# Optimization experiments

Hardware: AMD Instinct MI355X
Metric: run time of the kernel (lower is better)

Reference implementation:

```python
import jax, jax.numpy as jnp
import numpy as np

B, T, D_MODEL = 2, 1024, 1024
HEAD_DIM = 128
NUM_HEADS = D_MODEL // HEAD_DIM          # 8
EXPAND_V = 1
HEAD_V = HEAD_DIM * EXPAND_V             # 128
KEY_DIM = NUM_HEADS * HEAD_DIM           # 1024
VALUE_DIM = NUM_HEADS * HEAD_V           # 1024
CONV_SIZE = 4
NUM_LEVELS = int(np.log2(T)) + 1         # 11 Fenwick levels
EPS = 1e-5
SCALE = HEAD_DIM ** -0.5


def setup_inputs() -> dict:
    ks = jax.random.split(jax.random.key(0), 20)
    w = lambda i, shp: 0.02 * jax.random.normal(ks[i], shp, jnp.float32)
    return {
        'x': jax.random.normal(ks[0], (B, T, D_MODEL), jnp.float32),
        'cos': jax.random.normal(ks[1], (T, HEAD_DIM), jnp.float32),
        'sin': jax.random.normal(ks[2], (T, HEAD_DIM), jnp.float32),
        'Wq': w(3, (D_MODEL, KEY_DIM)),
        'Wk': w(4, (D_MODEL, KEY_DIM)),
        'Wv': w(5, (D_MODEL, VALUE_DIM)),
        'Wb': w(6, (D_MODEL, NUM_HEADS)),
        'Wa': w(7, (D_MODEL, NUM_HEADS)),
        'Wl': w(8, (D_MODEL, NUM_HEADS * NUM_LEVELS)),
        'Wg': w(9, (D_MODEL, VALUE_DIM)),
        'Wo': w(10, (VALUE_DIM, D_MODEL)),
        'conv_q': 0.2 * jax.random.normal(ks[11], (KEY_DIM, CONV_SIZE), jnp.float32),
        'conv_k': 0.2 * jax.random.normal(ks[12], (KEY_DIM, CONV_SIZE), jnp.float32),
        'conv_v': 0.2 * jax.random.normal(ks[13], (VALUE_DIM, CONV_SIZE), jnp.float32),
        'A_log': jnp.log(jax.random.uniform(ks[14], (NUM_HEADS,), jnp.float32, 1.0, 16.0)),
        'dt_bias': jnp.log(jnp.expm1(jax.random.uniform(ks[15], (NUM_HEADS,), jnp.float32, 0.001, 0.1))),
        'norm_w': jnp.ones((HEAD_V,), jnp.float32),
    }


def _dwconv_silu(x, w):
    # causal depthwise conv1d (ShortConvolution, activation=silu). x:[B,T,C], w:[C,K]
    xp = jnp.pad(x, ((0, 0), (CONV_SIZE - 1, 0), (0, 0)))
    y = jax.lax.conv_general_dilated(xp, w.T[:, None, :], (1,), 'VALID',
                                     dimension_numbers=('NHC', 'HIO', 'NHC'),
                                     feature_group_count=w.shape[0])
    return jax.nn.silu(y)


def _l2norm(x):
    return x * jax.lax.rsqrt(jnp.sum(x * x, -1, keepdims=True) + 1e-6)


def _levels():
    # Fenwick-tree level of token s (0-indexed) in the prefix decomposition at time t:
    # level(t,s) = floor(log2((t+1) XOR s)) for s <= t.
    n = jnp.arange(1, T + 1, dtype=jnp.int32)[:, None]
    s = jnp.arange(T, dtype=jnp.int32)[None, :]
    xval = jnp.maximum(jnp.bitwise_xor(n, s), 1)
    lev = jnp.floor(jnp.log2(xval.astype(jnp.float32))).astype(jnp.int32)
    return jnp.clip(lev, 0, NUM_LEVELS - 1)  # [T,T]


def _forward(x, Wq, Wk, Wv, Wb, Wa, Wl, Wg, Wo, conv_q, conv_k, conv_v, A_log, dt_bias, norm_w):
    # projections + short conv + silu, split heads -> [B,H,T,d]
    q = _dwconv_silu(x @ Wq, conv_q).reshape(B, T, NUM_HEADS, HEAD_DIM).transpose(0, 2, 1, 3)
    k = _dwconv_silu(x @ Wk, conv_k).reshape(B, T, NUM_HEADS, HEAD_DIM).transpose(0, 2, 1, 3)
    v = _dwconv_silu(x @ Wv, conv_v).reshape(B, T, NUM_HEADS, HEAD_V).transpose(0, 2, 1, 3)
    q = _l2norm(q) * SCALE
    k = _l2norm(k)
    beta = jax.nn.sigmoid(x @ Wb).transpose(0, 2, 1)                      # [B,H,T]
    g = -jnp.exp(A_log) * jax.nn.softplus(x @ Wa + dt_bias)              # [B,T,H] log-decay per step
    gc = jnp.cumsum(g.transpose(0, 2, 1), axis=-1)                        # [B,H,T]
    lam = jax.nn.sigmoid(x @ Wl).reshape(B, T, NUM_HEADS, NUM_LEVELS).transpose(0, 2, 1, 3)  # [B,H,T,L]

    idx = jnp.arange(T)
    causal = idx[:, None] >= idx[None, :]
    strict = idx[:, None] > idx[None, :]
    # stable decay matrix D[t,s] = exp(gc_t - gc_s) <= 1 for s <= t
    logD = gc[..., :, None] - gc[..., None, :]
    Dm = jnp.exp(jnp.where(causal, logD, -jnp.inf))                       # [B,H,T,T]

    # WY / UT transform of the gated delta rule:
    #   u_t = beta_t * v_t - beta_t * sum_{s<t} (k_t . k_s) exp(gc_t-gc_s) u_s
    Akk = jnp.einsum('bhtd,bhsd->bhts', k, k) * Dm * strict
    u = jax.scipy.linalg.solve_triangular(beta[..., None] * Akk,
                                          beta[..., None] * v,
                                          lower=True, unit_diagonal=True)  # [B,H,T,dv]

    # log-linear (hierarchical) readout: o_t = sum_s lam_t[level(t,s)] * (q_t.k_s) D[t,s] * u_s
    P = jnp.einsum('bhtd,bhsd->bhts', q, k) * Dm
    M = jnp.take_along_axis(lam, _levels()[None, None], axis=3)           # [B,H,T,T]
    o = jnp.einsum('bhts,bhsd->bhtd', P * M, u).transpose(0, 2, 1, 3)      # [B,T,H,dv]

    # gated RMSNorm output gate, then output projection
    gate = (x @ Wg).reshape(B, T, NUM_HEADS, HEAD_V)
    o = o * jax.lax.rsqrt(jnp.mean(o * o, -1, keepdims=True) + EPS) * norm_w * jax.nn.silu(gate)
    return o.reshape(B, T, VALUE_DIM) @ Wo


def reference(x, cos, sin, Wq, Wk, Wv, Wb, Wa, Wl, Wg, Wo, conv_q, conv_k, conv_v, A_log, dt_bias, norm_w):
    # cos/sin are accepted (block signature) but unused, matching the source module.
    return _forward(x, Wq, Wk, Wv, Wb, Wa, Wl, Wg, Wo, conv_q, conv_k, conv_v, A_log, dt_bias, norm_w)
```

## Files before the change

### kernel.cpp

```cpp
#include <hip/hip_runtime.h>
#include <hip/hip_bf16.h>
#include <math.h>

#define SCALE_Q 0.08838834764831845f

typedef __bf16 bf16x8 __attribute__((ext_vector_type(8)));
typedef float f32x4 __attribute__((ext_vector_type(4)));

static __device__ __forceinline__ float sigm(float x){ return 1.f/(1.f+__expf(-x)); }
static __device__ __forceinline__ ushort f2b(float v){
  __hip_bfloat16 t = __float2bfloat16(v);
  return __builtin_bit_cast(ushort, t);
}
static __device__ __forceinline__ float b2f(ushort u){
  unsigned v = (unsigned)u << 16; return __builtin_bit_cast(float, v);
}

__global__ __launch_bounds__(256) void prep_all(const float* __restrict__ Wq,
    const float* __restrict__ Wk, const float* __restrict__ Wv,
    const float* __restrict__ Wg, const float* __restrict__ Wo,
    const float* __restrict__ X, const float* __restrict__ Wb,
    const float* __restrict__ Wa, const float* __restrict__ Wl,
    ushort* __restrict__ Wt4, ushort* __restrict__ Wot,
    ushort* __restrict__ x16, float* __restrict__ Wsm)
{
  int z = blockIdx.z;
  int tid = threadIdx.x;
  int flat = blockIdx.y * 32 + blockIdx.x;
  if (z < 5) {
    __shared__ float tile[32][36];
    const float* W = (z==0)?Wq:(z==1)?Wk:(z==2)?Wv:(z==3)?Wg:Wo;
    ushort* Wt = (z<4)? (Wt4 + (size_t)z*1048576) : Wot;
    int n0 = blockIdx.x*32, k0 = blockIdx.y*32;
    int r = tid >> 3, c4 = (tid & 7) << 2;
    *(float4*)&tile[r][c4] = *(const float4*)&W[(size_t)(k0 + r)*1024 + n0 + c4];
    __syncthreads();
    ushort4 o;
    o.x = f2b(tile[c4+0][r]); o.y = f2b(tile[c4+1][r]);
    o.z = f2b(tile[c4+2][r]); o.w = f2b(tile[c4+3][r]);
    *(ushort4*)&Wt[(size_t)(n0 + r)*1024 + k0 + c4] = o;
  } else if (z < 7) {
    int idx = (z-5)*262144 + flat*256 + tid;
    float4 v = *(const float4*)&X[(size_t)idx*4];
    ushort4 o; o.x=f2b(v.x); o.y=f2b(v.y); o.z=f2b(v.z); o.w=f2b(v.w);
    *(ushort4*)&x16[(size_t)idx*4] = o;
  } else {
    int idx = flat*256 + tid;
    if (idx < 1024*104) {
      int k = idx / 104, c = idx % 104;
      float v = (c < 8) ? Wb[k*8+c] : (c < 16) ? Wa[k*8+(c-8)] : Wl[k*88+(c-16)];
      Wsm[idx] = v;
    }
  }
}

__global__ __launch_bounds__(256) void gemm_bf16(const ushort* __restrict__ A,
    const ushort* __restrict__ Bt, void* __restrict__ C0, float* __restrict__ C1,
    int M, int N, int K, int nsplit, int ld0, int ld1, int c0bf16)
{
  __shared__ ushort As[3][128*32];
  __shared__ ushort Bs[3][128*32];
  int tid = threadIdx.x;
  int gx = gridDim.x;
  int nwg = gx * gridDim.y;
  int id = blockIdx.y * gx + blockIdx.x;
  int id2 = (id & 7) * (nwg >> 3) + (id >> 3);
  int bm = (id2 / gx) * 128, bn = (id2 % gx) * 128;
  int wave = tid >> 6, lane = tid & 63;
  int wm = (wave >> 1) * 64, wn = (wave & 1) * 64;
  int l16 = lane & 15, kh = lane >> 4;
  f32x4 acc[4][4] = {};
  int rowA0 = tid >> 2, boA = (tid & 3) * 16;
  int niter = K >> 5;

  #pragma unroll
  for (int s = 0; s < 2; ++s) {
    int k0 = s << 5;
    #pragma unroll
    for (int j = 0; j < 2; ++j) {
      int row = rowA0 + j*64;
      const char* gA = (const char*)A + (((size_t)(bm+row)*K + k0)*2 + boA);
      const char* gB = (const char*)Bt + (((size_t)(bn+row)*K + k0)*2 + boA);
      __builtin_amdgcn_global_load_lds((const __attribute__((address_space(1))) unsigned*)gA,
        (__attribute__((address_space(3))) unsigned*)((char*)&As[s][0] + row*64 + boA), 16, 0, 0);
      __builtin_amdgcn_global_load_lds((const __attribute__((address_space(1))) unsigned*)gB,
        (__attribute__((address_space(3))) unsigned*)((char*)&Bs[s][0] + row*64 + boA), 16, 0, 0);
    }
  }
  asm volatile("s_waitcnt vmcnt(4)" ::: "memory");
  __builtin_amdgcn_s_barrier();
  __builtin_amdgcn_sched_barrier(0);
  for (int i = 0; i < niter; ++i) {
    int cur = i % 3;
    if (i + 2 < niter) {
      int k0 = (i+2) << 5;
      int nb = (i+2) % 3;
      char* al = (char*)&As[nb][0];
      char* bl = (char*)&Bs[nb][0];
      #pragma unroll
      for (int j = 0; j < 2; ++j) {
        int row = rowA0 + j*64;
        const char* gA = (const char*)A + (((size_t)(bm+row)*K + k0)*2 + boA);
        const char* gB = (const char*)Bt + (((size_t)(bn+row)*K + k0)*2 + boA);
        __builtin_amdgcn_global_load_lds((const __attribute__((address_space(1))) unsigned*)gA,
          (__attribute__((address_space(3))) unsigned*)(al + row*64 + boA), 16, 0, 0);
        __builtin_amdgcn_global_load_lds((const __attribute__((address_space(1))) unsigned*)gB,
          (__attribute__((address_space(3))) unsigned*)(bl + row*64 + boA), 16, 0, 0);
      }
    }
    bf16x8 af[4], bfr[4];
    #pragma unroll
    for (int ii = 0; ii < 4; ++ii)
      af[ii] = *(bf16x8*)((char*)&As[cur][0] + (wm + ii*16 + l16)*64 + kh*16);
    #pragma unroll
    for (int j = 0; j < 4; ++j)
      bfr[j] = *(bf16x8*)((char*)&Bs[cur][0] + (wn + j*16 + l16)*64 + kh*16);
    #pragma unroll
    for (int ii = 0; ii < 4; ++ii)
      #pragma unroll
      for (int j = 0; j < 4; ++j)
        acc[ii][j] = __builtin_amdgcn_mfma_f32_16x16x32_bf16(af[ii], bfr[j], acc[ii][j], 0, 0, 0);
    if (i + 1 < niter) {
      if (i + 2 < niter) {
        asm volatile("s_waitcnt vmcnt(4) lgkmcnt(0)" ::: "memory");
      } else {
        asm volatile("s_waitcnt vmcnt(0) lgkmcnt(0)" ::: "memory");
      }
      __builtin_amdgcn_s_barrier();
      __builtin_amdgcn_sched_barrier(0);
    }
  }
  int rg = lane >> 4;
  #pragma unroll
  for (int i = 0; i < 4; ++i) {
    #pragma unroll
    for (int j = 0; j < 4; ++j) {
      int col = bn + wn + j*16 + l16;
      #pragma unroll
      for (int r = 0; r < 4; ++r) {
        int row = bm + wm + i*16 + rg*4 + r;
        float v = acc[i][j][r];
        if (col < nsplit) {
          if (c0bf16) ((ushort*)C0)[(size_t)row*ld0 + col] = f2b(v);
          else        ((float*)C0)[(size_t)row*ld0 + col] = v;
        } else C1[(size_t)row*ld1 + (col - nsplit)] = v;
      }
    }
  }
}

__global__ __launch_bounds__(256) void skinny104(const float* __restrict__ X,
    const float* __restrict__ Wsm, float* __restrict__ part)
{
  __shared__ float XL[64][132];
  __shared__ float WsL[128][112];
  int tid = threadIdx.x;
  int m0 = blockIdx.x << 6;
  int k0 = blockIdx.y << 7;
  #pragma unroll
  for (int j = 0; j < 8; ++j) {
    int s = tid + j*256;
    int row = s >> 5, c4 = (s & 31) << 2;
    *(float4*)&XL[row][c4] = *(const float4*)&X[(size_t)(m0 + row)*1024 + k0 + c4];
  }
  {
    int k = tid >> 1, c = 104 + ((tid & 1) << 2);
    *(float4*)&WsL[k][c] = (float4){0.f,0.f,0.f,0.f};
  }
  {
    int k = tid >> 1, cb = (tid & 1) * 52;
    #pragma unroll
    for (int j = 0; j < 13; ++j) {
      *(float4*)&WsL[k][cb + j*4] = *(const float4*)&Wsm[(size_t)(k0 + k)*104 + cb + j*4];
    }
  }
  __syncthreads();
  int row = tid >> 2, cq = tid & 3;
  int cbase = cq * 28;
  f32x4 acc[7] = {};
  const float* xrow = &XL[row][0];
  #pragma unroll 4
  for (int k = 0; k < 128; ++k) {
    float xv = xrow[k];
    const f32x4* wr = (const f32x4*)&WsL[k][cbase];
    #pragma unroll
    for (int j = 0; j < 7; ++j) acc[j] += xv * wr[j];
  }
  float* pr = &part[((size_t)blockIdx.y*2048 + m0 + row)*104 + cbase];
  int nst = (cq == 3) ? 5 : 7;
  for (int j = 0; j < nst; ++j) *(f32x4*)&pr[j*4] = acc[j];
}

__global__ __launch_bounds__(256) void reduce8(const float* __restrict__ part,
    float* __restrict__ xs)
{
  int idx = blockIdx.x*256 + threadIdx.x;
  float s = 0.f;
  #pragma unroll
  for (int i = 0; i < 8; ++i) s += part[(size_t)i*212992 + idx];
  xs[idx] = s;
}

__global__ __launch_bounds__(256) void conv_fused(const ushort* __restrict__ Xall,
    const float* __restrict__ Wq, const float* __restrict__ Wk, const float* __restrict__ Wv,
    float* __restrict__ kbf, float* __restrict__ vbf,
    ushort* __restrict__ qb16, ushort* __restrict__ kb16, int ldx)
{
  int mode = blockIdx.y;
  const float* W = (mode==0)?Wq:(mode==1)?Wk:Wv;
  const ushort* X = Xall + mode*1024;
  int row = blockIdx.x;
  int b = row >> 10, t = row & 1023;
  int tid = threadIdx.x;
  int c0 = tid << 2;
  float w[4][4];
  #pragma unroll
  for (int c = 0; c < 4; ++c) {
    float4 wv = *(const float4*)&W[(c0 + c)*4];
    w[c][0]=wv.x; w[c][1]=wv.y; w[c][2]=wv.z; w[c][3]=wv.w;
  }
  float acc[4] = {0.f,0.f,0.f,0.f};
  #pragma unroll
  for (int j = 0; j < 4; ++j) {
    int tt = t - 3 + j;
    if (tt >= 0) {
      ushort4 xv = *(const ushort4*)&X[(size_t)(b*1024 + tt)*ldx + c0];
      acc[0] += w[0][j]*b2f(xv.x); acc[1] += w[1][j]*b2f(xv.y);
      acc[2] += w[2][j]*b2f(xv.z); acc[3] += w[3][j]*b2f(xv.w);
    }
  }
  #pragma unroll
  for (int c = 0; c < 4; ++c) acc[c] *= sigm(acc[c]);
  if (mode < 2) {
    float ss = acc[0]*acc[0]+acc[1]*acc[1]+acc[2]*acc[2]+acc[3]*acc[3];
    ss += __shfl_xor(ss, 1); ss += __shfl_xor(ss, 2); ss += __shfl_xor(ss, 4);
    ss += __shfl_xor(ss, 8); ss += __shfl_xor(ss, 16);
    float r = rsqrtf(ss + 1e-6f);
    if (mode == 0) r *= SCALE_Q;
    acc[0]*=r; acc[1]*=r; acc[2]*=r; acc[3]*=r;
  }
  size_t o = (size_t)(b*1024 + t)*1024 + c0;
  if (mode == 1) {
    float4 yv; yv.x=acc[0]; yv.y=acc[1]; yv.z=acc[2]; yv.w=acc[3];
    *(float4*)&kbf[o] = yv;
  } else if (mode == 2) {
    float4 yv; yv.x=acc[0]; yv.y=acc[1]; yv.z=acc[2]; yv.w=acc[3];
    *(float4*)&vbf[o] = yv;
  }
  if (mode == 0) {
    ushort4 yb; yb.x=f2b(acc[0]); yb.y=f2b(acc[1]); yb.z=f2b(acc[2]); yb.w=f2b(acc[3]);
    *(ushort4*)&qb16[o] = yb;
  } else if (mode == 1) {
    ushort4 yb; yb.x=f2b(acc[0]); yb.y=f2b(acc[1]); yb.z=f2b(acc[2]); yb.w=f2b(acc[3]);
    *(ushort4*)&kb16[o] = yb;
  }
}

__global__ __launch_bounds__(256) void gc2(const float* __restrict__ xs,
    const float* __restrict__ A_log, const float* __restrict__ dt_bias,
    float* __restrict__ gc)
{
  int bh = blockIdx.x, b = bh >> 3, h = bh & 7;
  __shared__ float sc[256];
  int tid = threadIdx.x;
  float aexp = __expf(A_log[h]), db = dt_bias[h];
  int t0 = tid*4;
  float g[4], csum = 0.f;
  #pragma unroll
  for (int z = 0; z < 4; ++z) {
    float zv = xs[(size_t)(b*1024 + t0 + z)*104 + 8 + h] + db;
    float sp = (zv > 20.f) ? zv : log1pf(__expf(zv));
    csum += -aexp*sp;
    g[z] = csum;
  }
  sc[tid] = csum;
  __syncthreads();
  for (int ofs = 1; ofs < 256; ofs <<= 1) {
    float v = (tid >= ofs) ? sc[tid-ofs] : 0.f;
    __syncthreads();
    sc[tid] += v;
    __syncthreads();
  }
  float excl = sc[tid] - csum;
  #pragma unroll
  for (int z = 0; z < 4; ++z) gc[bh*1024 + t0 + z] = excl + g[z];
}

__global__ __launch_bounds__(256) void chunk_prep(const float* __restrict__ Kg,
    const float* __restrict__ Vg, const float* __restrict__ xs,
    const float* __restrict__ gcg, float* __restrict__ cw, ushort* __restrict__ cWk16,
    ushort* __restrict__ cKpT16, float* __restrict__ eD)
{
  int blk = blockIdx.x;
  int bh = blk >> 4, ck = blk & 15;
  int b = bh >> 3, h = bh & 7;
  int a = ck << 6;
  __shared__ float Kc[64][132];
  __shared__ float As[64][68];
  __shared__ float gcl[65];
  __shared__ float bl[64];
  __shared__ float egc[64];
  __shared__ float edt[64];
  int tid = threadIdx.x;
  for (int e = tid; e < 64*32; e += 256) {
    int t = e >> 5, c4 = (e & 31) << 2;
    *(float4*)&Kc[t][c4] = *(const float4*)&Kg[(size_t)(b*1024 + a + t)*1024 + h*128 + c4];
  }
  if (tid < 64) {
    gcl[tid] = gcg[bh*1024 + a + tid];
    bl[tid] = sigm(xs[(size_t)(b*1024 + a + tid)*104 + h]);
  }
  if (tid == 64) gcl[64] = (ck < 15) ? gcg[bh*1024 + a + 64] : 0.f;
  __syncthreads();
  if (tid < 64) {
    egc[tid] = __expf(gcl[tid] - gcl[0]);
    edt[tid] = (ck < 15) ? __expf(gcl[64] - gcl[tid]) : 0.f;
  }
  {
    int ti = tid >> 4, si = tid & 15;
    if (si <= ti) {
      float dot[4][4] = {};
      for (int kk = 0; kk < 128; kk += 4) {
        float4 kt[4], ks[4];
        #pragma unroll
        for (int z = 0; z < 4; ++z) kt[z] = *(float4*)&Kc[ti*4+z][kk];
        #pragma unroll
        for (int z = 0; z < 4; ++z) ks[z] = *(float4*)&Kc[si*4+z][kk];
        #pragma unroll
        for (int i = 0; i < 4; ++i)
          #pragma unroll
          for (int j = 0; j < 4; ++j)
            dot[i][j] += kt[i].x*ks[j].x + kt[i].y*ks[j].y + kt[i].z*ks[j].z + kt[i].w*ks[j].w;
      }
      #pragma unroll
      for (int i = 0; i < 4; ++i) {
        int t = ti*4 + i;
        #pragma unroll
        for (int j = 0; j < 4; ++j) {
          int s = si*4 + j;
          if (s < t) As[t][s] = bl[t]*dot[i][j]*__expf(gcl[t]-gcl[s]);
        }
      }
    }
  }
  __syncthreads();
  int c = tid;
  float u[64];
  if (c < 128) {
    #pragma unroll
    for (int t = 0; t < 64; ++t)
      u[t] = bl[t]*Vg[(size_t)(b*1024 + a + t)*1024 + h*128 + c];
  } else {
    int d = c - 128;
    #pragma unroll
    for (int t = 0; t < 64; ++t)
      u[t] = bl[t]*egc[t]*Kc[t][d];
  }
  #pragma unroll
  for (int t = 1; t < 64; ++t) {
    float acc = u[t];
    int s = 0;
    #pragma unroll
    for (; s + 4 <= t; s += 4) {
      float4 a4 = *(float4*)&As[t][s];
      acc -= a4.x*u[s] + a4.y*u[s+1] + a4.z*u[s+2] + a4.w*u[s+3];
    }
    #pragma unroll
    for (; s < t; ++s) acc -= As[t][s]*u[s];
    u[t] = acc;
  }
  size_t cbase = (size_t)blk*8192;
  if (c < 128) {
    #pragma unroll
    for (int t = 0; t < 64; ++t)
      cw[cbase + t*128 + c] = u[t];
  } else {
    int d = c - 128;
    #pragma unroll
    for (int t = 0; t < 64; ++t) {
      cWk16[cbase + t*128 + d] = f2b(-u[t]);
      cKpT16[cbase + d*64 + t] = f2b(Kc[t][d]*edt[t]);
    }
  }
  if (tid == 0) eD[blk] = (ck < 15) ? __expf(gcl[64]-gcl[0]) : 0.f;
}

__global__ __launch_bounds__(256) void chunk_scan6(const float* __restrict__ cw,
    const ushort* __restrict__ cWk16, const ushort* __restrict__ cKpT16,
    const float* __restrict__ eD, ushort* __restrict__ Ut)
{
  int blk = blockIdx.x;
  int slice = blk >> 4, bh = blk & 15;
  int e_base = slice << 3;
  __shared__ ushort Wks[2][8192];
  __shared__ ushort Kps[2][8192];
  __shared__ ushort StT[16*128];
  __shared__ ushort usT[16*64];
  __shared__ float  Stf[128*16];
  int tid = threadIdx.x;
  int wave = tid >> 6, lane = tid & 63;
  int l15 = lane & 15, kh = lane >> 4;
  for (int idx = tid; idx < 16*128; idx += 256) StT[idx] = 0;
  for (int idx = tid; idx < 16*64; idx += 256) usT[idx] = 0;
  for (int idx = tid; idx < 128*16; idx += 256) Stf[idx] = 0.f;

  int e = l15;
  int t0 = wave*16 + kh*4;
  int ci0 = bh << 4;
  f32x4 wcur = {0.f,0.f,0.f,0.f};
  if (e < 8) {
    #pragma unroll
    for (int r = 0; r < 4; ++r)
      wcur[r] = cw[(size_t)ci0*8192 + (t0+r)*128 + e_base + e];
  }
  {
    const char* wg = (const char*)(cWk16 + (size_t)ci0*8192);
    const char* kg = (const char*)(cKpT16 + (size_t)ci0*8192);
    #pragma unroll
    for (int j = 0; j < 4; ++j) {
      unsigned off = (j<<12) + (tid<<4);
      unsigned wrow = off >> 8, wslot = (off >> 4) & 15;
      unsigned wsrc = wrow*256 + ((wslot ^ (wrow & 15)) << 4);
      __builtin_amdgcn_global_load_lds((const __attribute__((address_space(1))) unsigned*)(wg + wsrc),
        (__attribute__((address_space(3))) unsigned*)((char*)&Wks[0][0] + off), 16, 0, 0);
      unsigned krow = off >> 7, kslot = (off >> 4) & 7;
      unsigned ksrc = krow*128 + ((kslot ^ (krow & 7)) << 4);
      __builtin_amdgcn_global_load_lds((const __attribute__((address_space(1))) unsigned*)(kg + ksrc),
        (__attribute__((address_space(3))) unsigned*)((char*)&Kps[0][0] + off), 16, 0, 0);
    }
  }
  __syncthreads();

  for (int i = 0; i < 16; ++i) {
    int ci = ci0 + i, a = i << 6, cur = i & 1;
    f32x4 wnext = {0.f,0.f,0.f,0.f};
    if (i < 15) {
      if (e < 8) {
        #pragma unroll
        for (int r = 0; r < 4; ++r)
          wnext[r] = cw[(size_t)(ci+1)*8192 + (t0+r)*128 + e_base + e];
      }
      const char* wg = (const char*)(cWk16 + (size_t)(ci+1)*8192);
      const char* kg = (const char*)(cKpT16 + (size_t)(ci+1)*8192);
      char* wl = (char*)&Wks[cur^1][0];
      char* kl = (char*)&Kps[cur^1][0];
      #pragma unroll
      for (int j = 0; j < 4; ++j) {
        unsigned off = (j<<12) + (tid<<4);
        unsigned wrow = off >> 8, wslot = (off >> 4) & 15;
        unsigned wsrc = wrow*256 + ((wslot ^ (wrow & 15)) << 4);
        __builtin_amdgcn_global_load_lds((const __attribute__((address_space(1))) unsigned*)(wg + wsrc),
          (__attribute__((address_space(3))) unsigned*)(wl + off), 16, 0, 0);
        unsigned krow = off >> 7, kslot = (off >> 4) & 7;
        unsigned ksrc = krow*128 + ((kslot ^ (krow & 7)) << 4);
        __builtin_amdgcn_global_load_lds((const __attribute__((address_space(1))) unsigned*)(kg + ksrc),
          (__attribute__((address_space(3))) unsigned*)(kl + off), 16, 0, 0);
      }
    }
    {
      f32x4 d = wcur;
      const char* wkb = (const char*)&Wks[cur][0];
      int arow = wave*16 + l15;
      #pragma unroll
      for (int ks = 0; ks < 4; ++ks) {
        bf16x8 afr = *(const bf16x8*)(wkb + arow*256 + (((ks*4 + kh) ^ l15) << 4));
        bf16x8 bfr = *(const bf16x8*)((const char*)StT + l15*256 + (((ks*4 + kh) ^ l15) << 4));
        d = __builtin_amdgcn_mfma_f32_16x16x32_bf16(afr, bfr, d, 0, 0, 0);
      }
      if (e < 8) {
        ushort4 uw;
        uw.x = f2b(d[0]); uw.y = f2b(d[1]); uw.z = f2b(d[2]); uw.w = f2b(d[3]);
        *(ushort4*)((char*)usT + e*128 + (((t0>>3) ^ (e&7)) << 4) + (t0&7)*2) = uw;
        *(ushort4*)&Ut[(size_t)(bh*128 + e_base + e)*1024 + a + t0] = uw;
      }
    }
    asm volatile("s_waitcnt lgkmcnt(0)" ::: "memory");
    __builtin_amdgcn_s_barrier();
    __builtin_amdgcn_sched_barrier(0);
    if (i < 15) {
      float ed = eD[ci];
      const char* kpb = (const char*)&Kps[cur][0];
      #pragma unroll
      for (int mt = 0; mt < 2; ++mt) {
        int krow = (wave*2 + mt)*16 + l15;
        int k0 = (wave*2 + mt)*16 + kh*4;
        f32x4 c;
        #pragma unroll
        for (int r = 0; r < 4; ++r) c[r] = ed * Stf[(k0+r)*16 + e];
        #pragma unroll
        for (int ts = 0; ts < 2; ++ts) {
          bf16x8 afr = *(const bf16x8*)(kpb + krow*128 + (((ts*4 + kh) ^ (krow&7)) << 4));
          bf16x8 bfr = *(const bf16x8*)((const char*)usT + l15*128 + (((ts*4 + kh) ^ (l15&7)) << 4));
          c = __builtin_amdgcn_mfma_f32_16x16x32_bf16(afr, bfr, c, 0, 0, 0);
        }
        #pragma unroll
        for (int r = 0; r < 4; ++r) Stf[(k0+r)*16 + e] = c[r];
        if (e < 8) {
          ushort4 sw;
          sw.x = f2b(c[0]); sw.y = f2b(c[1]); sw.z = f2b(c[2]); sw.w = f2b(c[3]);
          *(ushort4*)((char*)StT + e*256 + (((k0>>3) ^ e) << 4) + (k0&7)*2) = sw;
        }
      }
      wcur = wnext;
      asm volatile("s_waitcnt vmcnt(0) lgkmcnt(0)" ::: "memory");
      __builtin_amdgcn_s_barrier();
      __builtin_amdgcn_sched_barrier(0);
    }
  }
}

__global__ __launch_bounds__(256) void readout3(const ushort* __restrict__ Qb,
    const ushort* __restrict__ Kb, const ushort* __restrict__ Ut,
    const float* __restrict__ gcg, const float* __restrict__ xs,
    float* __restrict__ Og)
{
  int blk = blockIdx.x;
  int bh = blk >> 4, ic = blk & 15;
  int half = blockIdx.y;
  int b = bh >> 3, h = bh & 7;
  int tbase = ic << 6;
  __shared__ ushort Ks[2][8192];
  __shared__ ushort Us[2][8192];
  __shared__ ushort Pl[4][1024];
  __shared__ float lamS[64][12];
  int tid = threadIdx.x;
  int wave = tid >> 6, lane = tid & 63;
  int l15 = lane & 15, kh = lane >> 4;

  const char* kgb = (const char*)Kb + ((size_t)(b*1024)*1024 + h*128)*2;
  const char* ugb = (const char*)Ut + ((size_t)(bh*128)*1024)*2;

  for (int e = tid; e < 64*11; e += 256) {
    int t = e/11, l = e%11;
    lamS[t][l] = sigm(xs[(size_t)(b*1024+tbase+t)*104 + 16 + h*11 + l]);
  }
  int tl = kh*4;
  float gct_r[4];
  #pragma unroll
  for (int r = 0; r < 4; ++r) gct_r[r] = gcg[bh*1024 + tbase + wave*16 + tl + r];
  bf16x8 qf[4];
  {
    const ushort* qp = &Qb[(size_t)(b*1024 + tbase + wave*16 + l15)*1024 + h*128 + kh*8];
    #pragma unroll
    for (int kk = 0; kk < 4; ++kk) qf[kk] = *(const bf16x8*)(qp + kk*32);
  }

  f32x4 accO[8] = {};
  int nsteps = ic + 1;
  int jmid = (nsteps + 1) >> 1;
  int j0 = half ? jmid : 0;
  int j1 = half ? nsteps : jmid;
  ushort* Pw = &Pl[wave][0];

  if (j0 < j1) {
    {
      const char* kg = kgb + (size_t)(j0<<6)*2048;
      const char* ug = ugb + (size_t)(j0<<6)*2;
      #pragma unroll
      for (int it = 0; it < 4; ++it) {
        unsigned off = (it<<12) + (tid<<4);
        unsigned krow = off >> 8, kc = (off >> 4) & 15;
        unsigned ksrc = krow*2048 + ((kc ^ (krow & 15)) << 4);
        __builtin_amdgcn_global_load_lds((const __attribute__((address_space(1))) unsigned*)(kg + ksrc),
          (__attribute__((address_space(3))) unsigned*)((char*)&Ks[0][0] + off), 16, 0, 0);
        unsigned ud = off >> 7, uc = (off >> 4) & 7;
        unsigned usrc = ud*2048 + ((uc ^ (ud & 7)) << 4);
        __builtin_amdgcn_global_load_lds((const __attribute__((address_space(1))) unsigned*)(ug + usrc),
          (__attribute__((address_space(3))) unsigned*)((char*)&Us[0][0] + off), 16, 0, 0);
      }
    }
    __syncthreads();
    int cur = 0;
    for (int j = j0; j < j1; ++j) {
      int sbase = j << 6;
      if (j + 1 < j1) {
        const char* kg = kgb + (size_t)((j+1)<<6)*2048;
        const char* ug = ugb + (size_t)((j+1)<<6)*2;
        char* kl = (char*)&Ks[cur^1][0];
        char* ul = (char*)&Us[cur^1][0];
        #pragma unroll
        for (int it = 0; it < 4; ++it) {
          unsigned off = (it<<12) + (tid<<4);
          unsigned krow = off >> 8, kc = (off >> 4) & 15;
          unsigned ksrc = krow*2048 + ((kc ^ (krow & 15)) << 4);
          __builtin_amdgcn_global_load_lds((const __attribute__((address_space(1))) unsigned*)(kg + ksrc),
            (__attribute__((address_space(3))) unsigned*)(kl + off), 16, 0, 0);
          unsigned ud = off >> 7, uc = (off >> 4) & 7;
          unsigned usrc = ud*2048 + ((uc ^ (ud & 7)) << 4);
          __builtin_amdgcn_global_load_lds((const __attribute__((address_space(1))) unsigned*)(ug + usrc),
            (__attribute__((address_space(3))) unsigned*)(ul + off), 16, 0, 0);
        }
      }
      float gcs_r[4];
      #pragma unroll
      for (int jt = 0; jt < 4; ++jt)
        gcs_r[jt] = gcg[bh*1024 + sbase + jt*16 + l15];
      f32x4 accS[4] = {};
      const char* ksb = (const char*)&Ks[cur][0];
      #pragma unroll
      for (int jt = 0; jt < 4; ++jt) {
        int row = jt*16 + l15;
        int rsw = row & 15;
        #pragma unroll
        for (int kk = 0; kk < 4; ++kk) {
          bf16x8 kf = *(const bf16x8*)(ksb + row*256 + (((kk*4 + kh) ^ rsw) << 4));
          accS[jt] = __builtin_amdgcn_mfma_f32_16x16x32_bf16(qf[kk], kf, accS[jt], 0, 0, 0);
        }
      }
      #pragma unroll
      for (int jt = 0; jt < 4; ++jt) {
        int sg = sbase + jt*16 + l15;
        #pragma unroll
        for (int r = 0; r < 4; ++r) {
          int t_loc = tl + r;
          int tg = tbase + wave*16 + t_loc;
          float pv = 0.f;
          if (sg <= tg) {
            int lev = 31 - __clz((unsigned)((tg+1) ^ sg));
            lev = lev > 10 ? 10 : lev;
            pv = accS[jt][r] * __expf(gct_r[r] - gcs_r[jt]) * lamS[wave*16 + t_loc][lev];
          }
          int bo = (t_loc << 7) + ((jt*16 + l15) << 1);
          bo ^= (t_loc & 7) << 4;
          *(ushort*)((char*)Pw + bo) = f2b(pv);
        }
      }
      const char* usb = (const char*)&Us[cur][0];
      #pragma unroll
      for (int ks = 0; ks < 2; ++ks) {
        int bo = (l15 << 7) + ((ks*32 + kh*8) << 1);
        bo ^= (l15 & 7) << 4;
        bf16x8 pa = *(bf16x8*)((char*)Pw + bo);
        #pragma unroll
        for (int dt = 0; dt < 8; ++dt) {
          int d = dt*16 + l15;
          bf16x8 uf = *(const bf16x8*)(usb + d*128 + (((ks*4 + kh) ^ (d & 7)) << 4));
          accO[dt] = __builtin_amdgcn_mfma_f32_16x16x32_bf16(pa, uf, accO[dt], 0, 0, 0);
        }
      }
      __syncthreads();
      cur ^= 1;
    }
  }
  float* og = Og + (size_t)half*2097152;
  #pragma unroll
  for (int dt = 0; dt < 8; ++dt) {
    #pragma unroll
    for (int r = 0; r < 4; ++r) {
      int row = tbase + wave*16 + tl + r;
      og[(size_t)(b*1024 + row)*1024 + h*128 + dt*16 + l15] = accO[dt][r];
    }
  }
}

__global__ __launch_bounds__(64) void normgate(const float* __restrict__ O1,
    const float* __restrict__ O2, const float* __restrict__ G,
    const float* __restrict__ norm_w, ushort* __restrict__ Y)
{
  int row = blockIdx.x;
  int lane = threadIdx.x;
  size_t base = (size_t)(row >> 3)*1024 + (size_t)(row & 7)*128;
  float2 oa = *(const float2*)&O1[base + lane*2];
  float2 ob = *(const float2*)&O2[base + lane*2];
  float ox = oa.x + ob.x, oy = oa.y + ob.y;
  float ss = ox*ox + oy*oy;
  #pragma unroll
  for (int m = 1; m < 64; m <<= 1) ss += __shfl_xor(ss, m);
  float r = rsqrtf(ss * (1.f/128.f) + 1e-5f);
  float2 g = *(const float2*)&G[base + lane*2];
  ushort2 y;
  y.x = f2b(ox * r * norm_w[lane*2+0] * (g.x * sigm(g.x)));
  y.y = f2b(oy * r * norm_w[lane*2+1] * (g.y * sigm(g.y)));
  *(ushort2*)&Y[base + lane*2] = y;
}

extern "C" void kernel_launch(void* const* d_in, const int* in_sizes, int n_in,
                              void* d_out, int out_size, void* d_ws, size_t ws_size,
                              hipStream_t stream)
{
  const float* x    = (const float*)d_in[0];
  const float* Wq   = (const float*)d_in[3];
  const float* Wk   = (const float*)d_in[4];
  const float* Wv   = (const float*)d_in[5];
  const float* Wb   = (const float*)d_in[6];
  const float* Wa   = (const float*)d_in[7];
  const float* Wl   = (const float*)d_in[8];
  const float* Wg   = (const float*)d_in[9];
  const float* Wo   = (const float*)d_in[10];
  const float* cq   = (const float*)d_in[11];
  const float* ck   = (const float*)d_in[12];
  const float* cv   = (const float*)d_in[13];
  const float* A_log   = (const float*)d_in[14];
  const float* dt_bias = (const float*)d_in[15];
  const float* norm_w  = (const float*)d_in[16];
  float* out = (float*)d_out;

  float* p = (float*)d_ws;
  float* xqkv = p;  p += 6291456;
  float* xg   = p;  p += 2097152;
  float* kb   = p;  p += 2097152;
  float* vb   = p;  p += 2097152;
  float* o1   = p;  p += 2097152;
  float* o2   = p;  p += 2097152;
  float* xs   = p;  p += 212992;
  float* gc   = p;  p += 16384;
  float* eD   = p;  p += 256;
  ushort* x16 = (ushort*)p; p += 1048576;
  ushort* Wt4 = (ushort*)p; p += 2097152;
  ushort* Wot = (ushort*)p; p += 524288;
  float* Wsm  = p;  p += 106496;
  ushort* yb16= (ushort*)p; p += 1048576;
  ushort* qb16= (ushort*)p; p += 1048576;
  ushort* kb16= (ushort*)p; p += 1048576;
  ushort* ut16= (ushort*)p; p += 1048576;
  ushort* xqkv16 = (ushort*)xqkv;
  float* cw  = xqkv;
  ushort* cWk16  = (ushort*)(xqkv + 2097152);
  ushort* cKpT16 = (ushort*)(xqkv + 3145728);
  float* part = o1;

  dim3 blk(256);
  prep_all<<<dim3(32,32,8), blk, 0, stream>>>(Wq, Wk, Wv, Wg, Wo, x, Wb, Wa, Wl,
                                              Wt4, Wot, x16, Wsm);
  gemm_bf16<<<dim3(32,16), blk, 0, stream>>>(x16, Wt4, xqkv16, xg, 2048, 4096, 1024,
                                             3072, 3072, 1024, 1);
  skinny104<<<dim3(32,8), blk, 0, stream>>>(x, Wsm, part);
  reduce8<<<dim3(833), blk, 0, stream>>>(part, xs);
  conv_fused<<<dim3(2048,3), blk, 0, stream>>>(xqkv16, cq, ck, cv, kb, vb, qb16, kb16, 3072);
  gc2<<<dim3(16), blk, 0, stream>>>(xs, A_log, dt_bias, gc);
  chunk_prep<<<dim3(256), blk, 0, stream>>>(kb, vb, xs, gc, cw, cWk16, cKpT16, eD);
  chunk_scan6<<<dim3(256), blk, 0, stream>>>(cw, cWk16, cKpT16, eD, ut16);
  readout3<<<dim3(256,2), blk, 0, stream>>>(qb16, kb16, ut16, gc, xs, o1);
  normgate<<<dim3(16384), dim3(64), 0, stream>>>(o1, o2, xg, norm_w, yb16);
  gemm_bf16<<<dim3(8,16), blk, 0, stream>>>(yb16, Wot, out, out, 2048, 1024, 1024,
                                            1024, 1024, 1024, 0);
}
```

Before: 196.4 us.

## Fuse skinny projection with its reduction and store conv k/v only as bf16

The split-K skinny projection plus its separate reduce kernel is replaced by a single kernel in which each block holds 8 full rows of x in shared memory and walks all 1024 k values, writing xs directly. This drops one launch and the partial-sum buffer round trip, but the weights are now read from global memory in every block with less parallelism (256 blocks and a long serial k loop). The depthwise conv also stops writing fp32 k and v and writes only bf16 copies, which chunk_prep now reads and widens. This halves that traffic at the cost of bf16 rounding on k and v inside the chunk solve.

```diff
diff --git a/kernel.cpp b/kernel.cpp
--- a/kernel.cpp
+++ b/kernel.cpp
@@ -149,62 +149,38 @@
   }
 }
 
-__global__ __launch_bounds__(256) void skinny104(const float* __restrict__ X,
-    const float* __restrict__ Wsm, float* __restrict__ part)
-{
-  __shared__ float XL[64][132];
-  __shared__ float WsL[128][112];
+__global__ __launch_bounds__(256) void skinny104f(const float* __restrict__ X,
+    const float* __restrict__ Wsm, float* __restrict__ xs)
+{
+  __shared__ float XL[8][1032];
   int tid = threadIdx.x;
-  int m0 = blockIdx.x << 6;
-  int k0 = blockIdx.y << 7;
+  int m0 = blockIdx.x << 3;
   #pragma unroll
   for (int j = 0; j < 8; ++j) {
     int s = tid + j*256;
-    int row = s >> 5, c4 = (s & 31) << 2;
-    *(float4*)&XL[row][c4] = *(const float4*)&X[(size_t)(m0 + row)*1024 + k0 + c4];
-  }
-  {
-    int k = tid >> 1, c = 104 + ((tid & 1) << 2);
-    *(float4*)&WsL[k][c] = (float4){0.f,0.f,0.f,0.f};
-  }
-  {
-    int k = tid >> 1, cb = (tid & 1) * 52;
-    #pragma unroll
-    for (int j = 0; j < 13; ++j) {
-      *(float4*)&WsL[k][cb + j*4] = *(const float4*)&Wsm[(size_t)(k0 + k)*104 + cb + j*4];
-    }
+    int row = s >> 8, c4 = (s & 255) << 2;
+    *(float4*)&XL[row][c4] = *(const float4*)&X[(size_t)(m0 + row)*1024 + c4];
   }
   __syncthreads();
-  int row = tid >> 2, cq = tid & 3;
-  int cbase = cq * 28;
-  f32x4 acc[7] = {};
-  const float* xrow = &XL[row][0];
-  #pragma unroll 4
-  for (int k = 0; k < 128; ++k) {
-    float xv = xrow[k];
-    const f32x4* wr = (const f32x4*)&WsL[k][cbase];
-    #pragma unroll
-    for (int j = 0; j < 7; ++j) acc[j] += xv * wr[j];
-  }
-  float* pr = &part[((size_t)blockIdx.y*2048 + m0 + row)*104 + cbase];
-  int nst = (cq == 3) ? 5 : 7;
-  for (int j = 0; j < nst; ++j) *(f32x4*)&pr[j*4] = acc[j];
-}
-
-__global__ __launch_bounds__(256) void reduce8(const float* __restrict__ part,
-    float* __restrict__ xs)
-{
-  int idx = blockIdx.x*256 + threadIdx.x;
-  float s = 0.f;
-  #pragma unroll
-  for (int i = 0; i < 8; ++i) s += part[(size_t)i*212992 + idx];
-  xs[idx] = s;
+  int r = tid >> 5, lane = tid & 31;
+  float a0=0.f, a1=0.f, a2=0.f, a3=0.f;
+  const float* xr = &XL[r][0];
+  for (int k = 0; k < 1024; ++k) {
+    float xv = xr[k];
+    const float* wr = &Wsm[(size_t)k*104];
+    a0 += xv*wr[lane];
+    a1 += xv*wr[lane+32];
+    a2 += xv*wr[lane+64];
+    if (lane < 8) a3 += xv*wr[lane+96];
+  }
+  size_t o = (size_t)(m0 + r)*104;
+  xs[o+lane] = a0; xs[o+lane+32] = a1; xs[o+lane+64] = a2;
+  if (lane < 8) xs[o+lane+96] = a3;
 }
 
 __global__ __launch_bounds__(256) void conv_fused(const ushort* __restrict__ Xall,
     const float* __restrict__ Wq, const float* __restrict__ Wk, const float* __restrict__ Wv,
-    float* __restrict__ kbf, float* __restrict__ vbf,
-    ushort* __restrict__ qb16, ushort* __restrict__ kb16, int ldx)
+    ushort* __restrict__ qb16, ushort* __restrict__ kb16, ushort* __restrict__ vb16, int ldx)
 {
   int mode = blockIdx.y;
   const float* W = (mode==0)?Wq:(mode==1)?Wk:Wv;
@@ -240,20 +216,9 @@
     acc[0]*=r; acc[1]*=r; acc[2]*=r; acc[3]*=r;
   }
   size_t o = (size_t)(b*1024 + t)*1024 + c0;
-  if (mode == 1) {
-    float4 yv; yv.x=acc[0]; yv.y=acc[1]; yv.z=acc[2]; yv.w=acc[3];
-    *(float4*)&kbf[o] = yv;
-  } else if (mode == 2) {
-    float4 yv; yv.x=acc[0]; yv.y=acc[1]; yv.z=acc[2]; yv.w=acc[3];
-    *(float4*)&vbf[o] = yv;
-  }
-  if (mode == 0) {
-    ushort4 yb; yb.x=f2b(acc[0]); yb.y=f2b(acc[1]); yb.z=f2b(acc[2]); yb.w=f2b(acc[3]);
-    *(ushort4*)&qb16[o] = yb;
-  } else if (mode == 1) {
-    ushort4 yb; yb.x=f2b(acc[0]); yb.y=f2b(acc[1]); yb.z=f2b(acc[2]); yb.w=f2b(acc[3]);
-    *(ushort4*)&kb16[o] = yb;
-  }
+  ushort* Y = (mode==0)?qb16:(mode==1)?kb16:vb16;
+  ushort4 yb; yb.x=f2b(acc[0]); yb.y=f2b(acc[1]); yb.z=f2b(acc[2]); yb.w=f2b(acc[3]);
+  *(ushort4*)&Y[o] = yb;
 }
 
 __global__ __launch_bounds__(256) void gc2(const float* __restrict__ xs,
@@ -286,8 +251,8 @@
   for (int z = 0; z < 4; ++z) gc[bh*1024 + t0 + z] = excl + g[z];
 }
 
-__global__ __launch_bounds__(256) void chunk_prep(const float* __restrict__ Kg,
-    const float* __restrict__ Vg, const float* __restrict__ xs,
+__global__ __launch_bounds__(256) void chunk_prep(const ushort* __restrict__ Kg16,
+    const ushort* __restrict__ Vg16, const float* __restrict__ xs,
     const float* __restrict__ gcg, float* __restrict__ cw, ushort* __restrict__ cWk16,
     ushort* __restrict__ cKpT16, float* __restrict__ eD)
 {
@@ -304,7 +269,9 @@
   int tid = threadIdx.x;
   for (int e = tid; e < 64*32; e += 256) {
     int t = e >> 5, c4 = (e & 31) << 2;
-    *(float4*)&Kc[t][c4] = *(const float4*)&Kg[(size_t)(b*1024 + a + t)*1024 + h*128 + c4];
+    ushort4 kv = *(const ushort4*)&Kg16[(size_t)(b*1024 + a + t)*1024 + h*128 + c4];
+    Kc[t][c4+0] = b2f(kv.x); Kc[t][c4+1] = b2f(kv.y);
+    Kc[t][c4+2] = b2f(kv.z); Kc[t][c4+3] = b2f(kv.w);
   }
   if (tid < 64) {
     gcl[tid] = gcg[bh*1024 + a + tid];
@@ -349,7 +316,7 @@
   if (c < 128) {
     #pragma unroll
     for (int t = 0; t < 64; ++t)
-      u[t] = bl[t]*Vg[(size_t)(b*1024 + a + t)*1024 + h*128 + c];
+      u[t] = bl[t]*b2f(Vg16[(size_t)(b*1024 + a + t)*1024 + h*128 + c]);
   } else {
     int d = c - 128;
     #pragma unroll
@@ -698,8 +665,8 @@
   float* p = (float*)d_ws;
   float* xqkv = p;  p += 6291456;
   float* xg   = p;  p += 2097152;
-  float* kb   = p;  p += 2097152;
-  float* vb   = p;  p += 2097152;
+  float* kbu  = p;  p += 2097152;
+  float* vbu  = p;  p += 2097152;
   float* o1   = p;  p += 2097152;
   float* o2   = p;  p += 2097152;
   float* xs   = p;  p += 212992;
@@ -714,21 +681,21 @@
   ushort* kb16= (ushort*)p; p += 1048576;
   ushort* ut16= (ushort*)p; p += 1048576;
   ushort* xqkv16 = (ushort*)xqkv;
+  ushort* vb16 = (ushort*)vbu;
   float* cw  = xqkv;
   ushort* cWk16  = (ushort*)(xqkv + 2097152);
   ushort* cKpT16 = (ushort*)(xqkv + 3145728);
-  float* part = o1;
+  (void)kbu;
 
   dim3 blk(256);
   prep_all<<<dim3(32,32,8), blk, 0, stream>>>(Wq, Wk, Wv, Wg, Wo, x, Wb, Wa, Wl,
                                               Wt4, Wot, x16, Wsm);
   gemm_bf16<<<dim3(32,16), blk, 0, stream>>>(x16, Wt4, xqkv16, xg, 2048, 4096, 1024,
                                              3072, 3072, 1024, 1);
-  skinny104<<<dim3(32,8), blk, 0, stream>>>(x, Wsm, part);
-  reduce8<<<dim3(833), blk, 0, stream>>>(part, xs);
-  conv_fused<<<dim3(2048,3), blk, 0, stream>>>(xqkv16, cq, ck, cv, kb, vb, qb16, kb16, 3072);
+  skinny104f<<<dim3(256), blk, 0, stream>>>(x, Wsm, xs);
+  conv_fused<<<dim3(2048,3), blk, 0, stream>>>(xqkv16, cq, ck, cv, qb16, kb16, vb16, 3072);
   gc2<<<dim3(16), blk, 0, stream>>>(xs, A_log, dt_bias, gc);
-  chunk_prep<<<dim3(256), blk, 0, stream>>>(kb, vb, xs, gc, cw, cWk16, cKpT16, eD);
+  chunk_prep<<<dim3(256), blk, 0, stream>>>(kb16, vb16, xs, gc, cw, cWk16, cKpT16, eD);
   chunk_scan6<<<dim3(256), blk, 0, stream>>>(cw, cWk16, cKpT16, eD, ut16);
   readout3<<<dim3(256,2), blk, 0, stream>>>(qb16, kb16, ut16, gc, xs, o1);
   normgate<<<dim3(16384), dim3(64), 0, stream>>>(o1, o2, xg, norm_w, yb16);
```

Result: slower. 448.3 us (+128.3%).
